# Optimization experiments

Measured on AMD Instinct MI355X. Metric: run time of the kernel, lower is better.

The kernel has to match this reference:

```python
import jax, jax.numpy as jnp
import numpy as np

EPS = 1e-13

def masked_softmax(scores, mask):
    # scores: [B, Lq, Lk], mask: [B, Lk] (float 0/1)
    # ESIM masked_softmax: softmax(scores * mask), zero masked cols, renormalize.
    m = mask[:, None, :]
    p = jax.nn.softmax(scores * m, axis=-1)
    p = p * m
    return p / (jnp.sum(p, axis=-1, keepdims=True) + EPS)

def weighted_sum(tensor, weights, mask):
    # tensor: [B, Lk, D], weights: [B, Lq, Lk], mask: [B, Lq]
    ws = jnp.einsum('bqk,bkd->bqd', weights, tensor)
    return ws * mask[:, :, None]

def setup_inputs() -> dict:
    key = jax.random.key(0)
    B, Lp, Lh, D, Dg = 32, 192, 192, 1024, 1024
    ks = jax.random.split(key, 6)
    premise_batch = jax.random.normal(ks[0], (B, Lp, D), jnp.float32)
    hypothesis_batch = jax.random.normal(ks[1], (B, Lh, D), jnp.float32)
    encoded_graph_emb_p = jax.random.normal(ks[2], (B, Lp, Dg), jnp.float32)
    encoded_graph_emb_h = jax.random.normal(ks[3], (B, Lh, Dg), jnp.float32)
    # realistic padding masks: prefix of ones up to a random length
    lp = jax.random.randint(ks[4], (B,), Lp // 2, Lp + 1)
    lh = jax.random.randint(ks[5], (B,), Lh // 2, Lh + 1)
    premise_mask = (jnp.arange(Lp)[None, :] < lp[:, None]).astype(jnp.float32)
    hypothesis_mask = (jnp.arange(Lh)[None, :] < lh[:, None]).astype(jnp.float32)
    return {
        'premise_batch': premise_batch,
        'premise_mask': premise_mask,
        'hypothesis_batch': hypothesis_batch,
        'hypothesis_mask': hypothesis_mask,
        'encoded_graph_emb_p': encoded_graph_emb_p,
        'encoded_graph_emb_h': encoded_graph_emb_h,
    }

def reference(premise_batch, premise_mask, hypothesis_batch, hypothesis_mask,
              encoded_graph_emb_p, encoded_graph_emb_h):
    # [B, Lp, Lh]
    similarity_matrix = jnp.einsum('bpd,bhd->bph', premise_batch, hypothesis_batch)
    similarity_matrix_g = jnp.einsum('bpd,bhd->bph', encoded_graph_emb_p, encoded_graph_emb_h)

    prem_hyp_attn = masked_softmax(similarity_matrix, hypothesis_mask)
    hyp_prem_attn = masked_softmax(jnp.swapaxes(similarity_matrix, 1, 2), premise_mask)
    prem_hyp_attn_g = masked_softmax(similarity_matrix_g, hypothesis_mask)
    hyp_prem_attn_g = masked_softmax(jnp.swapaxes(similarity_matrix_g, 1, 2), premise_mask)

    tot_attn_p = prem_hyp_attn + prem_hyp_attn_g
    tot_attn_h = hyp_prem_attn + hyp_prem_attn_g

    attended_premises = weighted_sum(hypothesis_batch, tot_attn_p, premise_mask)
    attended_hypotheses = weighted_sum(premise_batch, tot_attn_h, hypothesis_mask)
    attended_premises_g = weighted_sum(encoded_graph_emb_h, prem_hyp_attn_g, premise_mask)
    attended_hypotheses_g = weighted_sum(encoded_graph_emb_p, hyp_prem_attn_g, hypothesis_mask)

    return (tot_attn_p, tot_attn_h, attended_premises, attended_premises_g,
            attended_hypotheses, attended_hypotheses_g, prem_hyp_attn,
            hyp_prem_attn, prem_hyp_attn_g, hyp_prem_attn_g)
```

## Files before the change

kernel.cpp:

```cpp
#include <hip/hip_runtime.h>

constexpr int Bb = 32;
constexpr int L  = 192;
constexpr int Dk = 1024;
constexpr size_t A1 = (size_t)Bb * L * L;
constexpr size_t C1 = (size_t)Bb * L * Dk;

typedef short bf16x8 __attribute__((ext_vector_type(8)));
typedef float f32x4  __attribute__((ext_vector_type(4)));
typedef unsigned short ushort_t;

__device__ __forceinline__ unsigned short f2bf(float x){
  unsigned u = __float_as_uint(x);
  u = (u + 0x7FFFu + ((u >> 16) & 1u)) >> 16;
  return (unsigned short)u;
}
__device__ __forceinline__ bf16x8 ldfrag(const unsigned short* p){
  return *reinterpret_cast<const bf16x8*>(p);
}
__device__ __forceinline__ unsigned pack_hi16(unsigned ua, unsigned ub){
  return __builtin_amdgcn_perm(ua, ub, 0x03020706u);
}

__global__ __launch_bounds__(256) void sim_kernel(
    const float* __restrict__ P, const float* __restrict__ H,
    const float* __restrict__ Gp, const float* __restrict__ Gh,
    float* __restrict__ Sp, float* __restrict__ Sgp)
{
  const int orig = blockIdx.x;
  const int wg   = (orig & 7) * (1152 / 8) + (orig >> 3);
  const int tile = wg % 9;
  const int g    = wg / 9;
  const int ch   = g & 1;
  const int m    = (g >> 1) & 1;
  const int b    = g >> 2;

  const float* X = m ? Gp : P;
  const float* Y = m ? Gh : H;
  float* O = (m ? Sgp : Sp) + (size_t)ch * A1;

  const int ty = tile / 3, tx = tile % 3;
  const int brow = ty * 64, bcol = tx * 64;

  __shared__ unsigned short Ah[64][72], Al[64][72], Bh[64][72], Bl[64][72];

  const int tid  = threadIdx.x;
  const int r    = tid >> 2, q = tid & 3;
  const int lane = tid & 63, wid = tid >> 6;
  const int wm   = wid >> 1, wn = wid & 1;
  const int lr   = lane & 15, kg = lane >> 4;

  f32x4 acc[2][2] = {};

  const float* Xbase = X + (size_t)(b * L + brow + r) * Dk;
  const float* Ybase = Y + (size_t)(b * L + bcol + r) * Dk;
  const int k0beg = ch * 512;

  float4 xv[4], yv[4];

  auto load_regs = [&](int k0){
    #pragma unroll
    for (int j = 0; j < 4; ++j){
      const int c = (q + 4 * j) * 4;
      xv[j] = *reinterpret_cast<const float4*>(Xbase + k0 + c);
      yv[j] = *reinterpret_cast<const float4*>(Ybase + k0 + c);
    }
  };
  auto split_pack = [](const float4& v, uint2& hi, uint2& lo){
    unsigned ux = __float_as_uint(v.x), uy = __float_as_uint(v.y);
    unsigned uz = __float_as_uint(v.z), uw = __float_as_uint(v.w);
    float lx = v.x - __uint_as_float(ux & 0xFFFF0000u);
    float ly = v.y - __uint_as_float(uy & 0xFFFF0000u);
    float lz = v.z - __uint_as_float(uz & 0xFFFF0000u);
    float lw = v.w - __uint_as_float(uw & 0xFFFF0000u);
    hi.x = pack_hi16(ux, uy);
    hi.y = pack_hi16(uz, uw);
    lo.x = pack_hi16(__float_as_uint(lx), __float_as_uint(ly));
    lo.y = pack_hi16(__float_as_uint(lz), __float_as_uint(lw));
  };
  auto convert_store = [&](){
    #pragma unroll
    for (int j = 0; j < 4; ++j){
      const int c = (q + 4 * j) * 4;
      uint2 hi, lo;
      split_pack(xv[j], hi, lo);
      *reinterpret_cast<uint2*>(&Ah[r][c]) = hi;
      *reinterpret_cast<uint2*>(&Al[r][c]) = lo;
      split_pack(yv[j], hi, lo);
      *reinterpret_cast<uint2*>(&Bh[r][c]) = hi;
      *reinterpret_cast<uint2*>(&Bl[r][c]) = lo;
    }
  };

  load_regs(k0beg);
  convert_store();
  __syncthreads();

  for (int chunk = 0; chunk < 8; ++chunk){
    if (chunk < 7) load_regs(k0beg + (chunk + 1) * 64);

    #pragma unroll
    for (int kk = 0; kk < 64; kk += 32){
      const int ki = kk + kg * 8;
      bf16x8 ah[2], al[2], bh[2], bl[2];
      ah[0] = ldfrag(&Ah[wm * 32 +      lr][ki]);
      ah[1] = ldfrag(&Ah[wm * 32 + 16 + lr][ki]);
      al[0] = ldfrag(&Al[wm * 32 +      lr][ki]);
      al[1] = ldfrag(&Al[wm * 32 + 16 + lr][ki]);
      bh[0] = ldfrag(&Bh[wn * 32 +      lr][ki]);
      bh[1] = ldfrag(&Bh[wn * 32 + 16 + lr][ki]);
      bl[0] = ldfrag(&Bl[wn * 32 +      lr][ki]);
      bl[1] = ldfrag(&Bl[wn * 32 + 16 + lr][ki]);
      #pragma unroll
      for (int tm = 0; tm < 2; ++tm)
        #pragma unroll
        for (int tn = 0; tn < 2; ++tn){
          acc[tm][tn] = __builtin_amdgcn_mfma_f32_16x16x32_bf16(ah[tm], bh[tn], acc[tm][tn], 0, 0, 0);
          acc[tm][tn] = __builtin_amdgcn_mfma_f32_16x16x32_bf16(ah[tm], bl[tn], acc[tm][tn], 0, 0, 0);
          acc[tm][tn] = __builtin_amdgcn_mfma_f32_16x16x32_bf16(al[tm], bh[tn], acc[tm][tn], 0, 0, 0);
        }
    }
    __syncthreads();
    if (chunk < 7){
      convert_store();
      __syncthreads();
    }
  }

  float* Ob = O + (size_t)b * L * L;
  #pragma unroll
  for (int tm = 0; tm < 2; ++tm)
    #pragma unroll
    for (int tn = 0; tn < 2; ++tn){
      const int row0 = brow + wm * 32 + tm * 16 + kg * 4;
      const int col  = bcol + wn * 32 + tn * 16 + lr;
      #pragma unroll
      for (int i = 0; i < 4; ++i)
        Ob[(size_t)(row0 + i) * L + col] = acc[tm][tn][i];
    }
}

__global__ __launch_bounds__(256) void row_softmax(
    const float* __restrict__ Sp, const float* __restrict__ Sgp,
    const float* __restrict__ hmask,
    float* __restrict__ o7, float* __restrict__ o9, float* __restrict__ o1,
    ushort_t* __restrict__ w1, ushort_t* __restrict__ w9)
{
  const int b    = blockIdx.y;
  const int p    = blockIdx.x * 4 + (threadIdx.x >> 6);
  const int lane = threadIdx.x & 63;
  const size_t rowoff = ((size_t)b * L + p) * L;
  const float* sr  = Sp  + rowoff;
  const float* sgr = Sgp + rowoff;
  const float* mk  = hmask + (size_t)b * L;

  float m[3], v[3], vg[3];
  #pragma unroll
  for (int j = 0; j < 3; ++j){
    const int h = lane + 64 * j;
    const float mm = mk[h];
    m[j]  = mm;
    v[j]  = (sr [h] + sr [A1 + h]) * mm;
    vg[j] = (sgr[h] + sgr[A1 + h]) * mm;
  }
  float M  = fmaxf(fmaxf(v[0],  v[1]),  v[2]);
  float Mg = fmaxf(fmaxf(vg[0], vg[1]), vg[2]);
  #pragma unroll
  for (int off = 32; off; off >>= 1){
    M  = fmaxf(M,  __shfl_xor(M,  off));
    Mg = fmaxf(Mg, __shfl_xor(Mg, off));
  }
  float e[3], eg[3];
  float Z = 0.f, Zg = 0.f, Ein = 0.f, Eing = 0.f;
  #pragma unroll
  for (int j = 0; j < 3; ++j){
    e[j]  = expf(v[j]  - M);
    eg[j] = expf(vg[j] - Mg);
    Z  += e[j];  Ein  += m[j] * e[j];
    Zg += eg[j]; Eing += m[j] * eg[j];
  }
  #pragma unroll
  for (int off = 32; off; off >>= 1){
    Z    += __shfl_xor(Z,    off);
    Zg   += __shfl_xor(Zg,   off);
    Ein  += __shfl_xor(Ein,  off);
    Eing += __shfl_xor(Eing, off);
  }
  const float inv  = 1.f / (Ein  + 1e-13f * Z);
  const float invg = 1.f / (Eing + 1e-13f * Zg);
  #pragma unroll
  for (int j = 0; j < 3; ++j){
    const int h = lane + 64 * j;
    const float rj  = m[j] * e[j]  * inv;
    const float rgj = m[j] * eg[j] * invg;
    o7[rowoff + h] = rj;
    o9[rowoff + h] = rgj;
    o1[rowoff + h] = rj + rgj;
    if (w1){
      w1[rowoff + h] = f2bf(rj + rgj);
      w9[rowoff + h] = f2bf(rgj);
    }
  }
}

__global__ __launch_bounds__(256) void col_softmax(
    const float* __restrict__ Sp, const float* __restrict__ Sgp,
    const float* __restrict__ pmask,
    float* __restrict__ o8, float* __restrict__ o10, float* __restrict__ o2,
    ushort_t* __restrict__ w2, ushort_t* __restrict__ w10)
{
  __shared__ float Ts[192][33], Tg[192][33];
  const int b  = blockIdx.y;
  const int h0 = blockIdx.x * 32;
  const int tid = threadIdx.x;
  const size_t boff = (size_t)b * L * L;

  for (int i = tid; i < 192 * 8; i += 256){
    const int rr = i >> 3, qq = i & 7;
    const size_t base = boff + (size_t)rr * L + h0 + qq * 4;
    float4 a  = *reinterpret_cast<const float4*>(&Sp [base]);
    float4 a2 = *reinterpret_cast<const float4*>(&Sp [A1 + base]);
    float4 g  = *reinterpret_cast<const float4*>(&Sgp[base]);
    float4 g2 = *reinterpret_cast<const float4*>(&Sgp[A1 + base]);
    a.x += a2.x; a.y += a2.y; a.z += a2.z; a.w += a2.w;
    g.x += g2.x; g.y += g2.y; g.z += g2.z; g.w += g2.w;
    Ts[rr][qq*4+0] = a.x; Ts[rr][qq*4+1] = a.y; Ts[rr][qq*4+2] = a.z; Ts[rr][qq*4+3] = a.w;
    Tg[rr][qq*4+0] = g.x; Tg[rr][qq*4+1] = g.y; Tg[rr][qq*4+2] = g.z; Tg[rr][qq*4+3] = g.w;
  }
  __syncthreads();

  const int lane = tid & 63, wid = tid >> 6;
  const float* mk = pmask + (size_t)b * L;
  float m[3];
  #pragma unroll
  for (int j = 0; j < 3; ++j) m[j] = mk[lane + 64 * j];

  for (int c = 0; c < 8; ++c){
    const int hl = wid * 8 + c;
    const int h  = h0 + hl;
    float v[3], vg[3];
    #pragma unroll
    for (int j = 0; j < 3; ++j){
      v[j]  = Ts[lane + 64 * j][hl] * m[j];
      vg[j] = Tg[lane + 64 * j][hl] * m[j];
    }
    float M  = fmaxf(fmaxf(v[0],  v[1]),  v[2]);
    float Mg = fmaxf(fmaxf(vg[0], vg[1]), vg[2]);
    #pragma unroll
    for (int off = 32; off; off >>= 1){
      M  = fmaxf(M,  __shfl_xor(M,  off));
      Mg = fmaxf(Mg, __shfl_xor(Mg, off));
    }
    float e[3], eg[3];
    float Z = 0.f, Zg = 0.f, Ein = 0.f, Eing = 0.f;
    #pragma unroll
    for (int j = 0; j < 3; ++j){
      e[j]  = expf(v[j]  - M);
      eg[j] = expf(vg[j] - Mg);
      Z  += e[j];  Ein  += m[j] * e[j];
      Zg += eg[j]; Eing += m[j] * eg[j];
    }
    #pragma unroll
    for (int off = 32; off; off >>= 1){
      Z    += __shfl_xor(Z,    off);
      Zg   += __shfl_xor(Zg,   off);
      Ein  += __shfl_xor(Ein,  off);
      Eing += __shfl_xor(Eing, off);
    }
    const float inv  = 1.f / (Ein  + 1e-13f * Z);
    const float invg = 1.f / (Eing + 1e-13f * Zg);
    const size_t rowoff = ((size_t)b * L + h) * L;
    #pragma unroll
    for (int j = 0; j < 3; ++j){
      const int pp = lane + 64 * j;
      const float rj  = m[j] * e[j]  * inv;
      const float rgj = m[j] * eg[j] * invg;
      o8 [rowoff + pp] = rj;
      o10[rowoff + pp] = rgj;
      o2 [rowoff + pp] = rj + rgj;
      if (w2){
        w2 [rowoff + pp] = f2bf(rj + rgj);
        w10[rowoff + pp] = f2bf(rgj);
      }
    }
  }
}

__global__ __launch_bounds__(256) void wsum_kernel(
    const float* __restrict__ o1f, const float* __restrict__ o9f,
    const float* __restrict__ o2f, const float* __restrict__ o10f,
    const ushort_t* __restrict__ w1, const ushort_t* __restrict__ w9,
    const ushort_t* __restrict__ w2, const ushort_t* __restrict__ w10,
    const float* __restrict__ Pb, const float* __restrict__ Hb,
    const float* __restrict__ Gp, const float* __restrict__ Gh,
    const float* __restrict__ pmask, const float* __restrict__ hmask,
    float* __restrict__ o3, float* __restrict__ o4,
    float* __restrict__ o5, float* __restrict__ o6)
{
  const int orig = blockIdx.x;
  const int wg   = (orig & 7) * (2048 / 8) + (orig >> 3);
  const int dt   = wg & 15;
  const int gz   = wg >> 4;
  const int z    = gz & 3;
  const int b    = gz >> 2;
  const int d0   = dt * 64;

  const float* Wf; const ushort_t* Wh; const float* V; const float* qm; float* O;
  switch (z){
    case 0:  Wf = o1f;  Wh = w1;  V = Hb; qm = pmask; O = o3; break;
    case 1:  Wf = o9f;  Wh = w9;  V = Gh; qm = pmask; O = o4; break;
    case 2:  Wf = o2f;  Wh = w2;  V = Pb; qm = hmask; O = o5; break;
    default: Wf = o10f; Wh = w10; V = Gp; qm = hmask; O = o6; break;
  }

  __shared__ unsigned short Vt[64][68];

  const int tid  = threadIdx.x;
  const int r    = tid >> 2, q = tid & 3;
  const int lane = tid & 63, wv = tid >> 6;
  const int lr   = lane & 15, kg = lane >> 4;

  f32x4 acc[3][4] = {};

  for (int ck = 0; ck < 3; ++ck){
    const int k0 = ck * 64;

    bf16x8 afr[3][2];
    if (Wh){
      #pragma unroll
      for (int t = 0; t < 3; ++t)
        #pragma unroll
        for (int s = 0; s < 2; ++s){
          const int row = wv * 48 + t * 16 + lr;
          afr[t][s] = *reinterpret_cast<const bf16x8*>(
              Wh + ((size_t)b * L + row) * L + k0 + s * 32 + kg * 8);
        }
    } else {
      #pragma unroll
      for (int t = 0; t < 3; ++t)
        #pragma unroll
        for (int s = 0; s < 2; ++s){
          const int row = wv * 48 + t * 16 + lr;
          const float* wp = Wf + ((size_t)b * L + row) * L + k0 + s * 32 + kg * 8;
          float4 x0 = *reinterpret_cast<const float4*>(wp);
          float4 x1 = *reinterpret_cast<const float4*>(wp + 4);
          bf16x8 vv;
          vv[0] = f2bf(x0.x); vv[1] = f2bf(x0.y); vv[2] = f2bf(x0.z); vv[3] = f2bf(x0.w);
          vv[4] = f2bf(x1.x); vv[5] = f2bf(x1.y); vv[6] = f2bf(x1.z); vv[7] = f2bf(x1.w);
          afr[t][s] = vv;
        }
    }

    #pragma unroll
    for (int j = 0; j < 4; ++j){
      const int dcol = (q + 4 * j) * 4;
      float4 vvv = *reinterpret_cast<const float4*>(
          V + ((size_t)b * L + k0 + r) * Dk + d0 + dcol);
      Vt[dcol + 0][r] = (ushort_t)(__float_as_uint(vvv.x) >> 16);
      Vt[dcol + 1][r] = (ushort_t)(__float_as_uint(vvv.y) >> 16);
      Vt[dcol + 2][r] = (ushort_t)(__float_as_uint(vvv.z) >> 16);
      Vt[dcol + 3][r] = (ushort_t)(__float_as_uint(vvv.w) >> 16);
    }
    __syncthreads();

    #pragma unroll
    for (int s = 0; s < 2; ++s){
      const int ki = s * 32 + kg * 8;
      bf16x8 bfr[4];
      #pragma unroll
      for (int n = 0; n < 4; ++n)
        bfr[n] = ldfrag(&Vt[n * 16 + lr][ki]);
      #pragma unroll
      for (int t = 0; t < 3; ++t)
        #pragma unroll
        for (int n = 0; n < 4; ++n)
          acc[t][n] = __builtin_amdgcn_mfma_f32_16x16x32_bf16(afr[t][s], bfr[n], acc[t][n], 0, 0, 0);
    }
    __syncthreads();
  }

  #pragma unroll
  for (int t = 0; t < 3; ++t){
    const int row0 = wv * 48 + t * 16 + kg * 4;
    #pragma unroll
    for (int i = 0; i < 4; ++i){
      const int row  = row0 + i;
      const float mv = qm[(size_t)b * L + row];
      #pragma unroll
      for (int n = 0; n < 4; ++n)
        O[((size_t)b * L + row) * Dk + d0 + n * 16 + lr] = acc[t][n][i] * mv;
    }
  }
}

extern "C" void kernel_launch(void* const* d_in, const int* in_sizes, int n_in,
                              void* d_out, int out_size, void* d_ws, size_t ws_size,
                              hipStream_t stream) {
  const float* P  = (const float*)d_in[0];
  const float* pm = (const float*)d_in[1];
  const float* H  = (const float*)d_in[2];
  const float* hm = (const float*)d_in[3];
  const float* Gp = (const float*)d_in[4];
  const float* Gh = (const float*)d_in[5];
  float* out = (float*)d_out;

  float* o1  = out;
  float* o2  = out + A1;
  float* o3  = out + 2 * A1;
  float* o4  = o3 + C1;
  float* o5  = o3 + 2 * C1;
  float* o6  = o3 + 3 * C1;
  float* o7  = o3 + 4 * C1;
  float* o8  = o7 + A1;
  float* o9  = o7 + 2 * A1;
  float* o10 = o7 + 3 * A1;

  float* Sp  = o5;
  float* Sgp = o6;

  ushort_t* wb = (ws_size >= 4 * A1 * sizeof(ushort_t)) ? (ushort_t*)d_ws : nullptr;
  ushort_t* w1  = wb ? wb + 0 * A1 : nullptr;
  ushort_t* w9  = wb ? wb + 1 * A1 : nullptr;
  ushort_t* w2  = wb ? wb + 2 * A1 : nullptr;
  ushort_t* w10 = wb ? wb + 3 * A1 : nullptr;

  sim_kernel <<<dim3(1152),   256, 0, stream>>>(P, H, Gp, Gh, Sp, Sgp);
  row_softmax<<<dim3(48, 32), 256, 0, stream>>>(Sp, Sgp, hm, o7, o9, o1, w1, w9);
  col_softmax<<<dim3(6, 32),  256, 0, stream>>>(Sp, Sgp, pm, o8, o10, o2, w2, w10);
  wsum_kernel<<<dim3(2048),   256, 0, stream>>>(o1, o9, o2, o10, w1, w9, w2, w10,
                                                P, H, Gp, Gh, pm, hm, o3, o4, o5, o6);
}
```

Before: 90.64 us.

## Swizzle LDS tiles with XOR and software-pipeline weighted-sum global loads

Replaces padded shared-memory tiles with XOR-swizzled unpadded layouts in both the similarity GEMM and the weighted-sum kernel, to avoid LDS bank conflicts on fragment reads and transposed stores. The weighted-sum kernel is also unrolled into a double-buffered sequence: it prefetches the next K chunk of weights and V into registers while running MFMAs on the current chunk. This hides global load latency at the cost of more registers, which may reduce occupancy.

Result: slower. 95.31 us (+5.2%).

```diff
diff --git a/kernel.cpp b/kernel.cpp
--- a/kernel.cpp
+++ b/kernel.cpp
@@ -42,7 +42,7 @@
   const int ty = tile / 3, tx = tile % 3;
   const int brow = ty * 64, bcol = tx * 64;
 
-  __shared__ unsigned short Ah[64][72], Al[64][72], Bh[64][72], Bl[64][72];
+  __shared__ unsigned short Ah[64][64], Al[64][64], Bh[64][64], Bl[64][64];
 
   const int tid  = threadIdx.x;
   const int r    = tid >> 2, q = tid & 3;
@@ -81,14 +81,15 @@
   auto convert_store = [&](){
     #pragma unroll
     for (int j = 0; j < 4; ++j){
-      const int c = (q + 4 * j) * 4;
+      const int c  = (q + 4 * j) * 4;
+      const int cs = ((((c >> 3) ^ (r & 7)) << 3) | (c & 7));
       uint2 hi, lo;
       split_pack(xv[j], hi, lo);
-      *reinterpret_cast<uint2*>(&Ah[r][c]) = hi;
-      *reinterpret_cast<uint2*>(&Al[r][c]) = lo;
+      *reinterpret_cast<uint2*>(&Ah[r][cs]) = hi;
+      *reinterpret_cast<uint2*>(&Al[r][cs]) = lo;
       split_pack(yv[j], hi, lo);
-      *reinterpret_cast<uint2*>(&Bh[r][c]) = hi;
-      *reinterpret_cast<uint2*>(&Bl[r][c]) = lo;
+      *reinterpret_cast<uint2*>(&Bh[r][cs]) = hi;
+      *reinterpret_cast<uint2*>(&Bl[r][cs]) = lo;
     }
   };
 
@@ -96,21 +97,24 @@
   convert_store();
   __syncthreads();
 
+  const int rowA0 = wm * 32 + lr, rowA1 = rowA0 + 16;
+  const int rowB0 = wn * 32 + lr, rowB1 = rowB0 + 16;
+
   for (int chunk = 0; chunk < 8; ++chunk){
     if (chunk < 7) load_regs(k0beg + (chunk + 1) * 64);
 
     #pragma unroll
     for (int kk = 0; kk < 64; kk += 32){
-      const int ki = kk + kg * 8;
+      const int kb = (kk + kg * 8) >> 3;
       bf16x8 ah[2], al[2], bh[2], bl[2];
-      ah[0] = ldfrag(&Ah[wm * 32 +      lr][ki]);
-      ah[1] = ldfrag(&Ah[wm * 32 + 16 + lr][ki]);
-      al[0] = ldfrag(&Al[wm * 32 +      lr][ki]);
-      al[1] = ldfrag(&Al[wm * 32 + 16 + lr][ki]);
-      bh[0] = ldfrag(&Bh[wn * 32 +      lr][ki]);
-      bh[1] = ldfrag(&Bh[wn * 32 + 16 + lr][ki]);
-      bl[0] = ldfrag(&Bl[wn * 32 +      lr][ki]);
-      bl[1] = ldfrag(&Bl[wn * 32 + 16 + lr][ki]);
+      ah[0] = ldfrag(&Ah[rowA0][(kb ^ (rowA0 & 7)) << 3]);
+      ah[1] = ldfrag(&Ah[rowA1][(kb ^ (rowA1 & 7)) << 3]);
+      al[0] = ldfrag(&Al[rowA0][(kb ^ (rowA0 & 7)) << 3]);
+      al[1] = ldfrag(&Al[rowA1][(kb ^ (rowA1 & 7)) << 3]);
+      bh[0] = ldfrag(&Bh[rowB0][(kb ^ (rowB0 & 7)) << 3]);
+      bh[1] = ldfrag(&Bh[rowB1][(kb ^ (rowB1 & 7)) << 3]);
+      bl[0] = ldfrag(&Bl[rowB0][(kb ^ (rowB0 & 7)) << 3]);
+      bl[1] = ldfrag(&Bl[rowB1][(kb ^ (rowB1 & 7)) << 3]);
       #pragma unroll
       for (int tm = 0; tm < 2; ++tm)
         #pragma unroll
@@ -313,7 +317,7 @@
     default: Wf = o10f; Wh = w10; V = Gp; qm = hmask; O = o6; break;
   }
 
-  __shared__ unsigned short Vt[64][68];
+  __shared__ unsigned short Vt[64][64];
 
   const int tid  = threadIdx.x;
   const int r    = tid >> 2, q = tid & 3;
@@ -321,11 +325,10 @@
   const int lr   = lane & 15, kg = lane >> 4;
 
   f32x4 acc[3][4] = {};
-
-  for (int ck = 0; ck < 3; ++ck){
-    const int k0 = ck * 64;
-
-    bf16x8 afr[3][2];
+  bf16x8 afrA[3][2], afrB[3][2];
+  float4 vreg[4];
+
+  auto load_w = [&](int k0, bf16x8 (&afr)[3][2]){
     if (Wh){
       #pragma unroll
       for (int t = 0; t < 3; ++t)
@@ -350,34 +353,63 @@
           afr[t][s] = vv;
         }
     }
-
+  };
+  auto load_v = [&](int k0){
     #pragma unroll
     for (int j = 0; j < 4; ++j){
       const int dcol = (q + 4 * j) * 4;
-      float4 vvv = *reinterpret_cast<const float4*>(
+      vreg[j] = *reinterpret_cast<const float4*>(
           V + ((size_t)b * L + k0 + r) * Dk + d0 + dcol);
-      Vt[dcol + 0][r] = (ushort_t)(__float_as_uint(vvv.x) >> 16);
-      Vt[dcol + 1][r] = (ushort_t)(__float_as_uint(vvv.y) >> 16);
-      Vt[dcol + 2][r] = (ushort_t)(__float_as_uint(vvv.z) >> 16);
-      Vt[dcol + 3][r] = (ushort_t)(__float_as_uint(vvv.w) >> 16);
-    }
-    __syncthreads();
-
+    }
+  };
+  auto store_v = [&](){
+    #pragma unroll
+    for (int j = 0; j < 4; ++j){
+      const int dcol = (q + 4 * j) * 4;
+      unsigned t0 = __float_as_uint(vreg[j].x) >> 16;
+      unsigned t1 = __float_as_uint(vreg[j].y) >> 16;
+      unsigned t2 = __float_as_uint(vreg[j].z) >> 16;
+      unsigned t3 = __float_as_uint(vreg[j].w) >> 16;
+      #pragma unroll
+      for (int i = 0; i < 4; ++i){
+        const int d  = dcol + i;
+        const int cs = ((((r >> 3) ^ (d & 7)) << 3) | (r & 7));
+        Vt[d][cs] = (ushort_t)(i == 0 ? t0 : i == 1 ? t1 : i == 2 ? t2 : t3);
+      }
+    }
+  };
+  auto mfma_step = [&](bf16x8 (&afr)[3][2]){
     #pragma unroll
     for (int s = 0; s < 2; ++s){
-      const int ki = s * 32 + kg * 8;
+      const int kb = (s * 32 + kg * 8) >> 3;
       bf16x8 bfr[4];
       #pragma unroll
-      for (int n = 0; n < 4; ++n)
-        bfr[n] = ldfrag(&Vt[n * 16 + lr][ki]);
+      for (int n = 0; n < 4; ++n){
+        const int d = n * 16 + lr;
+        bfr[n] = ldfrag(&Vt[d][(kb ^ (d & 7)) << 3]);
+      }
       #pragma unroll
       for (int t = 0; t < 3; ++t)
         #pragma unroll
         for (int n = 0; n < 4; ++n)
           acc[t][n] = __builtin_amdgcn_mfma_f32_16x16x32_bf16(afr[t][s], bfr[n], acc[t][n], 0, 0, 0);
     }
-    __syncthreads();
-  }
+  };
+
+  load_w(0, afrA); load_v(0);
+  store_v();
+  __syncthreads();
+  load_w(64, afrB); load_v(64);
+  mfma_step(afrA);
+  __syncthreads();
+  store_v();
+  __syncthreads();
+  load_w(128, afrA); load_v(128);
+  mfma_step(afrB);
+  __syncthreads();
+  store_v();
+  __syncthreads();
+  mfma_step(afrA);
 
   #pragma unroll
   for (int t = 0; t < 3; ++t){
```
